# Optimization experiments

Measured on AMD Instinct MI355X. Metric: run time of the kernel, lower is better.

## Reference

```python
import jax, jax.numpy as jnp
import numpy as np

B, O, T = 32, 256, 1024
D_OBJ = 512      # obj_input_dim
D_PRED = 512     # predicate_input_dim
HID = 512        # hidden_dim
P_OUT = 512      # predicate_output_dim
OBJ_OUT = 512    # object_output_dim
N_PRED_TYPES = 50
ORIGINAL_EDGE = 0
TRANSITIVE_EDGE = 1


def setup_inputs() -> dict:
    key = jax.random.key(0)
    ks = jax.random.split(key, 16)

    def kaiming(k, fan_in, fan_out):
        return jax.random.normal(k, (fan_in, fan_out), jnp.float32) * np.sqrt(2.0 / fan_in)

    n1_in = 2 * D_OBJ + D_PRED            # 1536
    n1_out = 2 * HID + P_OUT              # 1536
    return {
        "obj_vecs": jax.random.normal(ks[0], (B, O, D_OBJ), jnp.float32),
        "pred_vecs": jax.random.normal(ks[1], (B, T, D_PRED), jnp.float32),
        "W1a": kaiming(ks[2], n1_in, HID), "b1a": jnp.zeros((HID,), jnp.float32),
        "W1b": kaiming(ks[3], HID, n1_out), "b1b": jnp.zeros((n1_out,), jnp.float32),
        "W2a": kaiming(ks[4], HID, HID), "b2a": jnp.zeros((HID,), jnp.float32),
        "W2b": kaiming(ks[5], HID, OBJ_OUT), "b2b": jnp.zeros((OBJ_OUT,), jnp.float32),
        "pt_weights": jax.random.normal(ks[6], (N_PRED_TYPES,), jnp.float32),
        "edges": jax.random.randint(ks[7], (B, T, 2), 0, O, jnp.int32),
        "pred_indicators": jax.random.randint(ks[8], (B, T), 0, 2, jnp.int32).astype(bool),
        "triplet_type": jax.random.randint(ks[9], (B, T), 0, 2, jnp.int32),
        "predicate_ids": jax.random.randint(ks[10], (B, T), 0, N_PRED_TYPES, jnp.int32),
    }


def reference(obj_vecs, pred_vecs, W1a, b1a, W1b, b1b, W2a, b2a, W2b, b2b,
              pt_weights, edges, pred_indicators, triplet_type, predicate_ids):
    s_idx = edges[:, :, 0]  # [B,T]
    o_idx = edges[:, :, 1]

    # gather subject/object vectors: [B,T,D]
    cur_s = jnp.take_along_axis(obj_vecs, s_idx[:, :, None], axis=1)
    cur_o = jnp.take_along_axis(obj_vecs, o_idx[:, :, None], axis=1)
    cur_t = jnp.concatenate([cur_s, pred_vecs, cur_o], axis=-1)  # [B,T,2D+Dp]

    # net1: Linear-ReLU-Linear-ReLU
    h = jax.nn.relu(cur_t @ W1a + b1a)
    new_t = jax.nn.relu(h @ W1b + b1b)  # [B,T,2*HID+P_OUT]

    # confidence weighting
    pt_pred = jax.nn.sigmoid(pt_weights)  # [N_PRED_TYPES]
    conf = ((triplet_type == ORIGINAL_EDGE).astype(jnp.float32)
            + (triplet_type == TRANSITIVE_EDGE).astype(jnp.float32) * pt_pred[predicate_ids])  # [B,T]
    new_t = new_t * conf[:, :, None]

    new_s = new_t[:, :, :HID]
    new_p = new_t[:, :, HID:HID + P_OUT]
    new_o = new_t[:, :, HID + P_OUT:]

    mask = pred_indicators.astype(jnp.float32)  # [B,T]

    def pool_one(si, oi, sv, ov, cf, m):
        # masked scatter-add (equivalent to torch boolean-masked scatter_add)
        sums = (jax.ops.segment_sum(sv * m[:, None], si, num_segments=O)
                + jax.ops.segment_sum(ov * m[:, None], oi, num_segments=O))  # [O,HID]
        w = cf * m
        counts = (jax.ops.segment_sum(w, si, num_segments=O)
                  + jax.ops.segment_sum(w, oi, num_segments=O))  # [O]
        nz = counts > 0
        return jnp.where(nz[:, None], sums / jnp.where(nz, counts, 1.0)[:, None], sums)

    pooled = jax.vmap(pool_one)(s_idx, o_idx, new_s, new_o, conf, mask)  # [B,O,HID]

    # net2: Linear-ReLU-Linear-ReLU
    h2 = jax.nn.relu(pooled @ W2a + b2a)
    new_obj = jax.nn.relu(h2 @ W2b + b2b)  # [B,O,OBJ_OUT]

    return new_obj, new_p
```

## Files before the change

kernel.cpp:

```cpp
#include <hip/hip_runtime.h>
#include <hip/hip_bf16.h>
#include <cstdint>
#include <cstddef>

#define DEV __device__ __forceinline__

typedef __attribute__((ext_vector_type(8))) short  s8v;
typedef __attribute__((ext_vector_type(4))) float  f4v;
typedef __attribute__((ext_vector_type(4))) uint32_t u4v;

DEV unsigned short f2bf(float x) {
  union { float f; uint32_t u; } v; v.f = x;
  uint32_t u = v.u + 0x7FFFu + ((v.u >> 16) & 1u);
  return (unsigned short)(u >> 16);
}
DEV uint32_t cvtpk2(float lo, float hi) {
  uint32_t r;
  asm("v_cvt_pk_bf16_f32 %0, %1, %2" : "=v"(r) : "v"(lo), "v"(hi));
  return r;
}
DEV unsigned short f2bf_fast(float x) { return (unsigned short)cvtpk2(x, 0.f); }
DEV float bf2f(unsigned short b) {
  union { uint32_t u; float f; } v; v.u = ((uint32_t)b) << 16;
  return v.f;
}

DEV void async_copy16(void* lds, const void* g) {
  typedef __attribute__((address_space(3))) uint32_t lds_t;
  typedef const __attribute__((address_space(1))) uint32_t g_t;
  __builtin_amdgcn_global_load_lds((g_t*)g, (lds_t*)lds, 16, 0, 0);
}

#define WAITV4()    asm volatile("s_waitcnt vmcnt(4)" ::: "memory")
#define WAITV0()    asm volatile("s_waitcnt vmcnt(0)" ::: "memory")
#define MEMFENCE()  asm volatile("" ::: "memory")

constexpr int Bc = 32, Oc = 256, Tc = 1024;
constexpr int BM = 128, BN = 128, BK = 64;
constexpr int CSR_CAP = 46;

DEV void swz_mn(int nyb, int* mb, int* nb) {
  const int nwg = gridDim.x * gridDim.y;
  const int w   = blockIdx.x + blockIdx.y * gridDim.x;
  const int cpx = nwg >> 3;
  const int s   = (w & 7) * cpx + (w >> 3);
  *mb = s / nyb;
  *nb = s % nyb;
}

__global__ __launch_bounds__(256)
void cvt_k(const float* __restrict__ in, unsigned short* __restrict__ outp, int n8)
{
  const int i = blockIdx.x * 256 + threadIdx.x;
  if (i >= n8) return;
  const f4v v0 = *(const f4v*)(in + (size_t)i * 8);
  const f4v v1 = *(const f4v*)(in + (size_t)i * 8 + 4);
  u4v pk;
  pk.x = cvtpk2(v0.x, v0.y);
  pk.y = cvtpk2(v0.z, v0.w);
  pk.z = cvtpk2(v1.x, v1.y);
  pk.w = cvtpk2(v1.z, v1.w);
  *(u4v*)(outp + (size_t)i * 8) = pk;
}

#define READ_A(QM, DST) do {                                                    \
    _Pragma("unroll")                                                           \
    for (int i = 0; i < 4; ++i) {                                               \
      const int row = wm * 128 + ((QM) * 4 + i) * 16 + (lane & 15);             \
      _Pragma("unroll")                                                         \
      for (int kk = 0; kk < 2; ++kk) {                                          \
        const int c = kk * 4 + (lane >> 4);                                     \
        DST[i][kk] = *(const s8v*)(Ab_ + row * 128 + ((c ^ (row & 7)) << 4));   \
      }                                                                         \
    }                                                                           \
  } while (0)

#define READ_B(QN, DST) do {                                                    \
    _Pragma("unroll")                                                           \
    for (int j = 0; j < 2; ++j) {                                               \
      const int row = wn * 64 + ((QN) * 2 + j) * 16 + (lane & 15);              \
      _Pragma("unroll")                                                         \
      for (int kk = 0; kk < 2; ++kk) {                                          \
        const int c = kk * 4 + (lane >> 4);                                     \
        DST[j][kk] = *(const s8v*)(Bb_ + row * 128 + ((c ^ (row & 7)) << 4));   \
      }                                                                         \
    }                                                                           \
  } while (0)

#define SYNC_MFMA(QM, QN, AF, BF) do {                                          \
    MEMFENCE();                                                                 \
    __builtin_amdgcn_s_barrier();                                               \
    asm volatile("s_waitcnt lgkmcnt(0)" ::: "memory");                          \
    __builtin_amdgcn_sched_barrier(0);                                          \
    __builtin_amdgcn_s_setprio(1);                                              \
    _Pragma("unroll")                                                           \
    for (int i = 0; i < 4; ++i)                                                 \
      _Pragma("unroll")                                                         \
      for (int j = 0; j < 2; ++j)                                               \
        _Pragma("unroll")                                                       \
        for (int kk = 0; kk < 2; ++kk)                                          \
          acc[(QM) * 4 + i][(QN) * 2 + j] =                                     \
            __builtin_amdgcn_mfma_f32_16x16x32_bf16(                            \
              AF[i][kk], BF[j][kk], acc[(QM) * 4 + i][(QN) * 2 + j], 0, 0, 0);  \
    __builtin_amdgcn_s_setprio(0);                                              \
  } while (0)

#define ENDPHASE() do { MEMFENCE(); __builtin_amdgcn_s_barrier(); } while (0)

#define KTILE_BODY() do {                                                       \
    const int par = t & 1, px = par ^ 1;                                        \
    const char* Ab_ = smem + par * 65536;                                       \
    const char* Bb_ = Ab_ + 32768;                                              \
    const bool s1 = (t + 1 < nk), s2 = (t + 2 < nk);                            \
                                                                        \
    READ_A(0, af); READ_B(0, bf0);                                              \
    if (s1) stageA(px, 1, t + 1);                                               \
    SYNC_MFMA(0, 0, af, bf0);                                                   \
    ENDPHASE();                                                                 \
                                                                        \
    READ_B(1, bf1);                                                             \
    if (s1) stageB(px, 1, t + 1);                                               \
    SYNC_MFMA(0, 1, af, bf1);                                                   \
    ENDPHASE();                                                                 \
                                                                        \
    READ_A(1, af);                                                              \
    if (s2) stageA(par, 0, t + 2);                                              \
    SYNC_MFMA(1, 1, af, bf1);                                                   \
    ENDPHASE();                                                                 \
                                                                        \
    if (s2) stageB(par, 0, t + 2);                                              \
    SYNC_MFMA(1, 0, af, bf0);                                                   \
    if (s2) { WAITV4(); } else if (s1) { WAITV0(); }                            \
    ENDPHASE();                                                                 \
  } while (0)

__global__ __launch_bounds__(512, 2)
void gemm8g_k(const unsigned short* __restrict__ objb,
              const unsigned short* __restrict__ predb,
              const int* __restrict__ edges,
              const unsigned short* __restrict__ Bt,
              const float* __restrict__ bias,
              unsigned short* __restrict__ outp)
{
  __shared__ __align__(16) char smem[131072];

  const int tid = threadIdx.x, lane = tid & 63, wave = tid >> 6;
  const int wm = wave >> 2, wn = wave & 3;
  int mb, nb; swz_mn(gridDim.y, &mb, &nb);
  const int m0 = mb * 256, n0 = nb * 256;
  const int rl  = tid >> 3;
  const int cs8 = ((lane & 7) ^ (lane >> 3)) * 8;
  const int rB0 = (rl >> 5) * 64 + (rl & 31);

  uint32_t offS[4], offP[4], offO[4];
  #pragma unroll
  for (int c2 = 0; c2 < 4; ++c2) {
    const int r = (c2 >> 1) * 128 + (c2 & 1) * 64 + rl;
    const int m = m0 + r;
    const int ob = (m >> 10) * Oc;
    offS[c2] = (uint32_t)((ob + edges[2 * m])     * 1024 + cs8 * 2);
    offO[c2] = (uint32_t)((ob + edges[2 * m + 1]) * 1024 + cs8 * 2);
    offP[c2] = (uint32_t)(m * 1024 + cs8 * 2);
  }
  const unsigned short* srcB = Bt + (size_t)(n0 + rB0) * 1536 + cs8;

  auto stageA = [&](int p, int qm, int kt) {
    const int reg = kt >> 3;
    const uint32_t koff = (uint32_t)(kt & 7) * 128u;
    #pragma unroll
    for (int s = 0; s < 2; ++s) {
      const int c2 = s * 2 + qm;
      const char* src;
      if (reg == 0)      src = (const char*)objb  + offS[c2] + koff;
      else if (reg == 1) src = (const char*)predb + offP[c2] + koff;
      else               src = (const char*)objb  + offO[c2] + koff;
      async_copy16(smem + p * 65536 + ((s * 128 + qm * 64 + wave * 8) << 7), src);
    }
  };
  auto stageB = [&](int p, int qn, int kt) {
    #pragma unroll
    for (int s = 0; s < 2; ++s)
      async_copy16(smem + p * 65536 + 32768 +
                     ((s * 128 + qn * 32 + (wave >> 2) * 64 + (wave & 3) * 8) << 7),
                   srcB + (size_t)(s * 128 + qn * 32) * 1536 + kt * 64);
  };

  f4v acc[8][4] = {};
  s8v af[4][2], bf0[2][2], bf1[2][2];
  constexpr int nk = 24;

  stageA(0, 0, 0); stageB(0, 0, 0); stageA(0, 1, 0); stageB(0, 1, 0);
  stageA(1, 0, 1); stageB(1, 0, 1);
  WAITV4();
  MEMFENCE();
  __builtin_amdgcn_s_barrier();

  for (int t = 0; t < nk; ++t) KTILE_BODY();

  const int cn = lane & 15, rq4 = (lane >> 4) * 4;
  #pragma unroll
  for (int f = 0; f < 8; ++f) {
    const int gr0 = m0 + wm * 128 + f * 16 + rq4;
    #pragma unroll
    for (int g = 0; g < 4; ++g) {
      const int gc = n0 + wn * 64 + g * 16 + cn;
      const float bv = bias[gc];
      #pragma unroll
      for (int r = 0; r < 4; ++r) {
        float val = acc[f][g][r] + bv;
        val = val > 0.f ? val : 0.f;
        outp[(size_t)(gr0 + r) * 512 + gc] = f2bf_fast(val);
      }
    }
  }
}

template<int EPI>
__global__ __launch_bounds__(256)
void gemm_k(const unsigned short* __restrict__ Abf,
            const unsigned short* __restrict__ Bt,
            const float* __restrict__ bias,
            const float* __restrict__ conf,
            unsigned short* __restrict__ out_bf,
            float* __restrict__ out_f32,
            int M, int N, int K)
{
  __shared__ __align__(16) char smem[BM * BK * 2 + BN * BK * 2];
  char* As = smem;
  char* Bs = smem + BM * BK * 2;

  const int tid  = threadIdx.x;
  const int lane = tid & 63;
  const int wave = tid >> 6;
  const int wm = wave >> 1, wn = wave & 1;
  int mb, nb; swz_mn(gridDim.y, &mb, &nb);
  const int m0 = mb * BM;
  const int n0 = nb * BN;

  f4v acc[4][4] = {};

  for (int k0 = 0; k0 < K; k0 += BK) {
    {
      const int r8 = lane >> 3;
      const int cs = (lane & 7) ^ r8;
      const unsigned short* src = Bt + (size_t)(n0 + wave * 32 + r8) * K + k0 + cs * 8;
      #pragma unroll
      for (int i = 0; i < 4; ++i)
        async_copy16(Bs + (wave * 32 + i * 8) * 128, src + (size_t)i * 8 * K);
      const unsigned short* srca = Abf + (size_t)(m0 + wave * 32 + r8) * K + k0 + cs * 8;
      #pragma unroll
      for (int i = 0; i < 4; ++i)
        async_copy16(As + (wave * 32 + i * 8) * 128, srca + (size_t)i * 8 * K);
    }
    __syncthreads();

    #pragma unroll
    for (int kk = 0; kk < 2; ++kk) {
      s8v af[4], bfv[4];
      #pragma unroll
      for (int i = 0; i < 4; ++i) {
        const int row = wm * 64 + i * 16 + (lane & 15);
        const int c = kk * 4 + (lane >> 4);
        af[i] = *(const s8v*)(As + row * 128 + ((c ^ (row & 7)) << 4));
      }
      #pragma unroll
      for (int j = 0; j < 4; ++j) {
        const int row = wn * 64 + j * 16 + (lane & 15);
        const int c = kk * 4 + (lane >> 4);
        bfv[j] = *(const s8v*)(Bs + row * 128 + ((c ^ (row & 7)) << 4));
      }
      #pragma unroll
      for (int i = 0; i < 4; ++i)
        #pragma unroll
        for (int j = 0; j < 4; ++j)
          acc[i][j] = __builtin_amdgcn_mfma_f32_16x16x32_bf16(af[i], bfv[j], acc[i][j], 0, 0, 0);
    }
    __syncthreads();
  }

  const int cn = lane & 15, rq4 = (lane >> 4) * 4;
  #pragma unroll
  for (int i = 0; i < 4; ++i) {
    const int gr0 = m0 + wm * 64 + i * 16 + rq4;
    #pragma unroll
    for (int j = 0; j < 4; ++j) {
      const int gc = n0 + wn * 64 + j * 16 + cn;
      const float bv = bias[gc];
      #pragma unroll
      for (int r = 0; r < 4; ++r) {
        float val = acc[i][j][r] + bv;
        val = val > 0.f ? val : 0.f;
        const int gr = gr0 + r;
        if (EPI == 0) out_bf[(size_t)gr * N + gc] = f2bf_fast(val);
        else if (EPI == 2) out_f32[(size_t)gr * N + gc] = val;
        else { out_f32[(size_t)gr * N + gc] = val * conf[gr]; }
      }
    }
  }
}

__global__ __launch_bounds__(256)
void gemm2so_k(const unsigned short* __restrict__ h,
               const int* __restrict__ torig,
               const float* __restrict__ confc,
               const unsigned short* __restrict__ W1bt,
               const float* __restrict__ b1b,
               const int* __restrict__ minfo,
               unsigned short* __restrict__ news_c,
               unsigned short* __restrict__ newo_c)
{
  const int Mp   = minfo[1];
  const int nact = (Mp >> 7) << 3;
  const int w    = blockIdx.x + blockIdx.y * gridDim.x;
  if (w >= nact) return;
  const int cpx = nact >> 3;
  const int s   = (w & 7) * cpx + (w >> 3);
  const int mb  = s >> 3, nb = s & 7;
  const int m0  = mb * BM;
  const int Mr  = minfo[0];

  __shared__ __align__(16) char smem[BM * BK * 2 + BN * BK * 2];
  char* As = smem;
  char* Bs = smem + BM * BK * 2;

  const int tid  = threadIdx.x;
  const int lane = tid & 63;
  const int wave = tid >> 6;
  const int wm = wave >> 1, wn = wave & 1;
  const int n0 = nb * BN;
  const int r8 = lane >> 3;
  const int cs8 = ((lane & 7) ^ r8) * 8;

  const unsigned short* aP[4];
  #pragma unroll
  for (int i = 0; i < 4; ++i) {
    int m = m0 + wave * 32 + i * 8 + r8;
    m = m < Mr ? m : Mr - 1;
    aP[i] = h + (size_t)torig[m] * 512 + cs8;
  }
  const int nrow0 = (nb < 4) ? n0 : n0 + 512;
  const unsigned short* bsrc = W1bt + (size_t)(nrow0 + wave * 32 + r8) * 512 + cs8;

  f4v acc[4][4] = {};

  for (int kt = 0; kt < 8; ++kt) {
    const int kin = kt * 64;
    #pragma unroll
    for (int i = 0; i < 4; ++i)
      async_copy16(Bs + (wave * 32 + i * 8) * 128, bsrc + (size_t)(i * 8) * 512 + kin);
    #pragma unroll
    for (int i = 0; i < 4; ++i)
      async_copy16(As + (wave * 32 + i * 8) * 128, aP[i] + kin);
    __syncthreads();

    #pragma unroll
    for (int kk = 0; kk < 2; ++kk) {
      s8v af[4], bfv[4];
      #pragma unroll
      for (int i = 0; i < 4; ++i) {
        const int row = wm * 64 + i * 16 + (lane & 15);
        const int c = kk * 4 + (lane >> 4);
        af[i] = *(const s8v*)(As + row * 128 + ((c ^ (row & 7)) << 4));
      }
      #pragma unroll
      for (int j = 0; j < 4; ++j) {
        const int row = wn * 64 + j * 16 + (lane & 15);
        const int c = kk * 4 + (lane >> 4);
        bfv[j] = *(const s8v*)(Bs + row * 128 + ((c ^ (row & 7)) << 4));
      }
      #pragma unroll
      for (int i = 0; i < 4; ++i)
        #pragma unroll
        for (int j = 0; j < 4; ++j)
          acc[i][j] = __builtin_amdgcn_mfma_f32_16x16x32_bf16(af[i], bfv[j], acc[i][j], 0, 0, 0);
    }
    __syncthreads();
  }

  const float* bb = b1b + ((nb < 4) ? n0 : 512 + n0);
  unsigned short* outp = (nb < 4) ? news_c : newo_c;
  const int c0 = (nb & 3) * 128;
  const int cn = lane & 15, rq4 = (lane >> 4) * 4;
  #pragma unroll
  for (int i = 0; i < 4; ++i) {
    const int gr0 = m0 + wm * 64 + i * 16 + rq4;
    #pragma unroll
    for (int j = 0; j < 4; ++j) {
      const int lc = wn * 64 + j * 16 + cn;
      const float bv = bb[lc];
      #pragma unroll
      for (int r = 0; r < 4; ++r) {
        const int gr = gr0 + r;
        float val = acc[i][j][r] + bv;
        val = val > 0.f ? val : 0.f;
        val *= confc[gr < Mr ? gr : 0];
        if (gr < Mr) outp[(size_t)gr * 512 + c0 + lc] = f2bf_fast(val);
      }
    }
  }
}

__global__ void tcvt_k(const float* __restrict__ W, unsigned short* __restrict__ Wt,
                       int K, int N)
{
  __shared__ float tile[32][33];
  const int k0 = blockIdx.x * 32, n0 = blockIdx.y * 32;
  const int tx = threadIdx.x, ty = threadIdx.y;
  #pragma unroll
  for (int i = 0; i < 32; i += 8)
    tile[ty + i][tx] = W[(size_t)(k0 + ty + i) * N + (n0 + tx)];
  __syncthreads();
  #pragma unroll
  for (int i = 0; i < 32; i += 8)
    Wt[(size_t)(n0 + ty + i) * K + (k0 + tx)] = f2bf(tile[tx][ty + i]);
}

__global__ void detect_k(const unsigned char* __restrict__ mb, int* __restrict__ flag)
{
  __shared__ int any;
  if (threadIdx.x == 0) any = 0;
  __syncthreads();
  int local = 0;
  for (int i = threadIdx.x; i < Bc * Tc; i += 256)
    if ((i & 3) && mb[i]) local = 1;
  if (local) atomicOr(&any, 1);
  __syncthreads();
  if (threadIdx.x == 0) *flag = any;
}

__global__ void prep_k(const int* __restrict__ tt, const int* __restrict__ pid,
                       const float* __restrict__ ptw, const int* __restrict__ edges,
                       const void* __restrict__ mask, const int* __restrict__ u8flag,
                       float* __restrict__ conf, int* __restrict__ se,
                       int* __restrict__ oe)
{
  const int m = blockIdx.x * 256 + threadIdx.x;
  const int t = tt[m];
  float c = 0.f;
  if (t == 0) c = 1.f;
  else if (t == 1) c = 1.f / (1.f + expf(-ptw[pid[m]]));
  conf[m] = c;
  bool mk;
  if (*u8flag) mk = ((const unsigned char*)mask)[m] != 0;
  else         mk = ((const int*)mask)[m] != 0;
  se[m] = mk ? edges[2 * m]     : -1;
  oe[m] = mk ? edges[2 * m + 1] : -1;
}

__global__ __launch_bounds__(1024)
void scan1_k(const int* __restrict__ se, int* __restrict__ bsum)
{
  const int m = blockIdx.x * 1024 + threadIdx.x;
  const unsigned long long bal = __ballot(se[m] >= 0);
  __shared__ int wc[16];
  if ((threadIdx.x & 63) == 0) wc[threadIdx.x >> 6] = (int)__popcll(bal);
  __syncthreads();
  if (threadIdx.x == 0) {
    int s = 0;
    #pragma unroll
    for (int i = 0; i < 16; ++i) s += wc[i];
    bsum[blockIdx.x] = s;
  }
}

__global__ void scan2_k(const int* __restrict__ bsum, int* __restrict__ boff,
                        int* __restrict__ minfo)
{
  if (threadIdx.x == 0) {
    int s = 0;
    for (int i = 0; i < 32; ++i) { boff[i] = s; s += bsum[i]; }
    minfo[0] = s;
    minfo[1] = (s + 127) & ~127;
  }
}

__global__ __launch_bounds__(1024)
void scan3_k(const int* __restrict__ se, const int* __restrict__ boff,
             const float* __restrict__ conf,
             int* __restrict__ torig, int* __restrict__ cmap,
             float* __restrict__ confc)
{
  const int m = blockIdx.x * 1024 + threadIdx.x;
  const int lane = threadIdx.x & 63, w = threadIdx.x >> 6;
  const bool mv = se[m] >= 0;
  const unsigned long long bal = __ballot(mv);
  __shared__ int wc[16];
  if (lane == 0) wc[w] = (int)__popcll(bal);
  __syncthreads();
  int woff = 0;
  for (int i = 0; i < w; ++i) woff += wc[i];
  if (mv) {
    const int c = boff[blockIdx.x] + woff +
                  (int)__popcll(bal & ((1ull << lane) - 1ull));
    torig[c] = m;
    cmap[m]  = c;
    confc[c] = conf[m];
  }
}

__global__ __launch_bounds__(256)
void csr2_k(const int* __restrict__ se, const int* __restrict__ oe,
            int* __restrict__ deg, int* __restrict__ slot)
{
  const int wid  = blockIdx.x * 4 + (threadIdx.x >> 6);
  const int b    = wid >> 8;
  const int u    = wid & 255;
  const int lane = threadIdx.x & 63;
  const int mb   = b * Tc;
  int* sl = slot + (size_t)wid * CSR_CAP;
  const unsigned long long lt = (1ull << lane) - 1ull;
  int cnt = 0;
  #pragma unroll 4
  for (int c = 0; c < 16; ++c) {
    const int t = c * 64 + lane;
    const int s = se[mb + t];
    const int o = oe[mb + t];
    const unsigned long long ms = __ballot(s == u);
    const unsigned long long mo = __ballot(o == u);
    if (s == u) {
      const int pos = cnt + (int)__popcll(ms & lt);
      if (pos < CSR_CAP) sl[pos] = 2 * t;
    }
    cnt += (int)__popcll(ms);
    if (o == u) {
      const int pos = cnt + (int)__popcll(mo & lt);
      if (pos < CSR_CAP) sl[pos] = 2 * t + 1;
    }
    cnt += (int)__popcll(mo);
  }
  if (lane == 0) deg[wid] = cnt < CSR_CAP ? cnt : CSR_CAP;
}

__global__ __launch_bounds__(256)
void pool2_k(const unsigned short* __restrict__ S, const unsigned short* __restrict__ Ov,
             const int* __restrict__ deg, const int* __restrict__ slot,
             const float* __restrict__ conf, const int* __restrict__ cmap,
             unsigned short* __restrict__ pooled)
{
  const int bo = blockIdx.x;
  const int b  = bo >> 8;
  const int u  = threadIdx.x;
  const int d  = deg[bo];
  const int* sl = slot + (size_t)bo * CSR_CAP;
  float a0 = 0.f, a1 = 0.f, w = 0.f;
  for (int i = 0; i < d; ++i) {
    const int e = sl[i];
    const int t = e >> 1;
    const int c = cmap[b * Tc + t];
    const unsigned short* row = ((e & 1) ? Ov : S) + (size_t)c * 512;
    const uint32_t pr = *(const uint32_t*)(row + 2 * u);
    a0 += bf2f((unsigned short)pr);
    a1 += bf2f((unsigned short)(pr >> 16));
    w  += conf[b * Tc + t];
  }
  const float denom = (w > 0.f) ? w : 1.f;
  const size_t ob = (size_t)bo * 512;
  *(uint32_t*)(pooled + ob + 2 * u) = cvtpk2(a0 / denom, a1 / denom);
}

extern "C" void kernel_launch(void* const* d_in, const int* in_sizes, int n_in,
                              void* d_out, int out_size, void* d_ws, size_t ws_size,
                              hipStream_t stream)
{
  const float* obj  = (const float*)d_in[0];
  const float* pred = (const float*)d_in[1];
  const float* W1a  = (const float*)d_in[2];
  const float* b1a  = (const float*)d_in[3];
  const float* W1b  = (const float*)d_in[4];
  const float* b1b  = (const float*)d_in[5];
  const float* W2a  = (const float*)d_in[6];
  const float* b2a  = (const float*)d_in[7];
  const float* W2b  = (const float*)d_in[8];
  const float* b2b  = (const float*)d_in[9];
  const float* ptw  = (const float*)d_in[10];
  const int*   edges = (const int*)d_in[11];
  const void*  mask  = d_in[12];
  const int*   tt    = (const int*)d_in[13];
  const int*   pid   = (const int*)d_in[14];
  float* out = (float*)d_out;

  char* ws = (char*)d_ws;
  unsigned short* W1at = (unsigned short*)(ws + 0);
  unsigned short* W1bt = (unsigned short*)(ws + 1572864);
  unsigned short* W2at = (unsigned short*)(ws + 3145728);
  unsigned short* W2bt = (unsigned short*)(ws + 3670016);
  int* deg  = (int*)(ws + 0);
  int* slot = (int*)(ws + 32768);
  unsigned short* h    = (unsigned short*)(ws + 4194304);
  unsigned short* pooled = h;
  unsigned short* h2   = (unsigned short*)(ws + 12582912);
  unsigned short* news = (unsigned short*)(ws + 37748736);
  unsigned short* newo = (unsigned short*)(ws + 71303168);
  unsigned short* objb = news;
  unsigned short* predb = (unsigned short*)(ws + 46137344);
  float* conf = (float*)(ws + 104857600);
  int*   se   = (int*)(ws + 104988672);
  int*   oe   = (int*)(ws + 105119744);
  int* u8flag = (int*)(ws + 105250816);

  char* sout = (char*)d_out;
  int*   torig = (int*)(sout + 0);
  int*   cmap  = (int*)(sout + 131072);
  float* confc = (float*)(sout + 262144);
  int*   bsum  = (int*)(sout + 393216);
  int*   boff  = (int*)(sout + 393344);
  int*   minfo = (int*)(sout + 393472);

  tcvt_k<<<dim3(48, 16), dim3(32, 8), 0, stream>>>(W1a, W1at, 1536, 512);
  tcvt_k<<<dim3(16, 48), dim3(32, 8), 0, stream>>>(W1b, W1bt, 512, 1536);
  tcvt_k<<<dim3(16, 16), dim3(32, 8), 0, stream>>>(W2a, W2at, 512, 512);
  tcvt_k<<<dim3(16, 16), dim3(32, 8), 0, stream>>>(W2b, W2bt, 512, 512);

  cvt_k<<<2048, 256, 0, stream>>>(obj,  objb,  Bc * Oc * 512 / 8);
  cvt_k<<<8192, 256, 0, stream>>>(pred, predb, Bc * Tc * 512 / 8);

  detect_k<<<1, 256, 0, stream>>>((const unsigned char*)mask, u8flag);
  prep_k<<<128, 256, 0, stream>>>(tt, pid, ptw, edges, mask, u8flag, conf, se, oe);

  scan1_k<<<32, 1024, 0, stream>>>(se, bsum);
  scan2_k<<<1, 64, 0, stream>>>(bsum, boff, minfo);
  scan3_k<<<32, 1024, 0, stream>>>(se, boff, conf, torig, cmap, confc);

  gemm8g_k<<<dim3(128, 2), 512, 0, stream>>>(objb, predb, edges, W1at, b1a, h);

  csr2_k<<<2048, 256, 0, stream>>>(se, oe, deg, slot);

  gemm_k<3><<<dim3(256, 4), 256, 0, stream>>>(
      h, W1bt + 512 * 512, b1b + 512, conf, nullptr, out + 4194304, 32768, 512, 512);

  gemm2so_k<<<dim3(256, 8), 256, 0, stream>>>(
      h, torig, confc, W1bt, b1b, minfo, news, newo);

  pool2_k<<<Bc * Oc, 256, 0, stream>>>(news, newo, deg, slot, conf, cmap, pooled);

  gemm_k<0><<<dim3(64, 4), 256, 0, stream>>>(
      pooled, W2at, b2a, nullptr, h2, nullptr, 8192, 512, 512);

  gemm_k<2><<<dim3(64, 4), 256, 0, stream>>>(
      h2, W2bt, b2b, nullptr, nullptr, out, 8192, 512, 512);
}
```

Measured before the change: 254.5 us.

## Precompute per-object projections to shrink first-layer GEMM from K=1536 to K=512

The first linear layer is split algebraically. The subject and object parts of W1a are applied once per object (8192 rows) in a separate GEMM that writes fp32 projections into scratch output space. A new fused GEMM then handles only the predicate part (K=512) and adds the gathered subject and object projections plus bias in its epilogue. This removes the gathered K=1536 GEMM over 32768 rows, but adds an extra kernel, fp32 gathers in the epilogue, and a simpler single-buffered GEMM in place of the hand-pipelined one.

```diff
diff --git a/kernel.cpp b/kernel.cpp
--- a/kernel.cpp
+++ b/kernel.cpp
@@ -30,10 +30,6 @@
   typedef const __attribute__((address_space(1))) uint32_t g_t;
   __builtin_amdgcn_global_load_lds((g_t*)g, (lds_t*)lds, 16, 0, 0);
 }
-
-#define WAITV4()    asm volatile("s_waitcnt vmcnt(4)" ::: "memory")
-#define WAITV0()    asm volatile("s_waitcnt vmcnt(0)" ::: "memory")
-#define MEMFENCE()  asm volatile("" ::: "memory")
 
 constexpr int Bc = 32, Oc = 256, Tc = 1024;
 constexpr int BM = 128, BN = 128, BK = 64;
@@ -63,158 +59,6 @@
   *(u4v*)(outp + (size_t)i * 8) = pk;
 }
 
-#define READ_A(QM, DST) do {                                                    \
-    _Pragma("unroll")                                                           \
-    for (int i = 0; i < 4; ++i) {                                               \
-      const int row = wm * 128 + ((QM) * 4 + i) * 16 + (lane & 15);             \
-      _Pragma("unroll")                                                         \
-      for (int kk = 0; kk < 2; ++kk) {                                          \
-        const int c = kk * 4 + (lane >> 4);                                     \
-        DST[i][kk] = *(const s8v*)(Ab_ + row * 128 + ((c ^ (row & 7)) << 4));   \
-      }                                                                         \
-    }                                                                           \
-  } while (0)
-
-#define READ_B(QN, DST) do {                                                    \
-    _Pragma("unroll")                                                           \
-    for (int j = 0; j < 2; ++j) {                                               \
-      const int row = wn * 64 + ((QN) * 2 + j) * 16 + (lane & 15);              \
-      _Pragma("unroll")                                                         \
-      for (int kk = 0; kk < 2; ++kk) {                                          \
-        const int c = kk * 4 + (lane >> 4);                                     \
-        DST[j][kk] = *(const s8v*)(Bb_ + row * 128 + ((c ^ (row & 7)) << 4));   \
-      }                                                                         \
-    }                                                                           \
-  } while (0)
-
-#define SYNC_MFMA(QM, QN, AF, BF) do {                                          \
-    MEMFENCE();                                                                 \
-    __builtin_amdgcn_s_barrier();                                               \
-    asm volatile("s_waitcnt lgkmcnt(0)" ::: "memory");                          \
-    __builtin_amdgcn_sched_barrier(0);                                          \
-    __builtin_amdgcn_s_setprio(1);                                              \
-    _Pragma("unroll")                                                           \
-    for (int i = 0; i < 4; ++i)                                                 \
-      _Pragma("unroll")                                                         \
-      for (int j = 0; j < 2; ++j)                                               \
-        _Pragma("unroll")                                                       \
-        for (int kk = 0; kk < 2; ++kk)                                          \
-          acc[(QM) * 4 + i][(QN) * 2 + j] =                                     \
-            __builtin_amdgcn_mfma_f32_16x16x32_bf16(                            \
-              AF[i][kk], BF[j][kk], acc[(QM) * 4 + i][(QN) * 2 + j], 0, 0, 0);  \
-    __builtin_amdgcn_s_setprio(0);                                              \
-  } while (0)
-
-#define ENDPHASE() do { MEMFENCE(); __builtin_amdgcn_s_barrier(); } while (0)
-
-#define KTILE_BODY() do {                                                       \
-    const int par = t & 1, px = par ^ 1;                                        \
-    const char* Ab_ = smem + par * 65536;                                       \
-    const char* Bb_ = Ab_ + 32768;                                              \
-    const bool s1 = (t + 1 < nk), s2 = (t + 2 < nk);                            \
-                                                                        \
-    READ_A(0, af); READ_B(0, bf0);                                              \
-    if (s1) stageA(px, 1, t + 1);                                               \
-    SYNC_MFMA(0, 0, af, bf0);                                                   \
-    ENDPHASE();                                                                 \
-                                                                        \
-    READ_B(1, bf1);                                                             \
-    if (s1) stageB(px, 1, t + 1);                                               \
-    SYNC_MFMA(0, 1, af, bf1);                                                   \
-    ENDPHASE();                                                                 \
-                                                                        \
-    READ_A(1, af);                                                              \
-    if (s2) stageA(par, 0, t + 2);                                              \
-    SYNC_MFMA(1, 1, af, bf1);                                                   \
-    ENDPHASE();                                                                 \
-                                                                        \
-    if (s2) stageB(par, 0, t + 2);                                              \
-    SYNC_MFMA(1, 0, af, bf0);                                                   \
-    if (s2) { WAITV4(); } else if (s1) { WAITV0(); }                            \
-    ENDPHASE();                                                                 \
-  } while (0)
-
-__global__ __launch_bounds__(512, 2)
-void gemm8g_k(const unsigned short* __restrict__ objb,
-              const unsigned short* __restrict__ predb,
-              const int* __restrict__ edges,
-              const unsigned short* __restrict__ Bt,
-              const float* __restrict__ bias,
-              unsigned short* __restrict__ outp)
-{
-  __shared__ __align__(16) char smem[131072];
-
-  const int tid = threadIdx.x, lane = tid & 63, wave = tid >> 6;
-  const int wm = wave >> 2, wn = wave & 3;
-  int mb, nb; swz_mn(gridDim.y, &mb, &nb);
-  const int m0 = mb * 256, n0 = nb * 256;
-  const int rl  = tid >> 3;
-  const int cs8 = ((lane & 7) ^ (lane >> 3)) * 8;
-  const int rB0 = (rl >> 5) * 64 + (rl & 31);
-
-  uint32_t offS[4], offP[4], offO[4];
-  #pragma unroll
-  for (int c2 = 0; c2 < 4; ++c2) {
-    const int r = (c2 >> 1) * 128 + (c2 & 1) * 64 + rl;
-    const int m = m0 + r;
-    const int ob = (m >> 10) * Oc;
-    offS[c2] = (uint32_t)((ob + edges[2 * m])     * 1024 + cs8 * 2);
-    offO[c2] = (uint32_t)((ob + edges[2 * m + 1]) * 1024 + cs8 * 2);
-    offP[c2] = (uint32_t)(m * 1024 + cs8 * 2);
-  }
-  const unsigned short* srcB = Bt + (size_t)(n0 + rB0) * 1536 + cs8;
-
-  auto stageA = [&](int p, int qm, int kt) {
-    const int reg = kt >> 3;
-    const uint32_t koff = (uint32_t)(kt & 7) * 128u;
-    #pragma unroll
-    for (int s = 0; s < 2; ++s) {
-      const int c2 = s * 2 + qm;
-      const char* src;
-      if (reg == 0)      src = (const char*)objb  + offS[c2] + koff;
-      else if (reg == 1) src = (const char*)predb + offP[c2] + koff;
-      else               src = (const char*)objb  + offO[c2] + koff;
-      async_copy16(smem + p * 65536 + ((s * 128 + qm * 64 + wave * 8) << 7), src);
-    }
-  };
-  auto stageB = [&](int p, int qn, int kt) {
-    #pragma unroll
-    for (int s = 0; s < 2; ++s)
-      async_copy16(smem + p * 65536 + 32768 +
-                     ((s * 128 + qn * 32 + (wave >> 2) * 64 + (wave & 3) * 8) << 7),
-                   srcB + (size_t)(s * 128 + qn * 32) * 1536 + kt * 64);
-  };
-
-  f4v acc[8][4] = {};
-  s8v af[4][2], bf0[2][2], bf1[2][2];
-  constexpr int nk = 24;
-
-  stageA(0, 0, 0); stageB(0, 0, 0); stageA(0, 1, 0); stageB(0, 1, 0);
-  stageA(1, 0, 1); stageB(1, 0, 1);
-  WAITV4();
-  MEMFENCE();
-  __builtin_amdgcn_s_barrier();
-
-  for (int t = 0; t < nk; ++t) KTILE_BODY();
-
-  const int cn = lane & 15, rq4 = (lane >> 4) * 4;
-  #pragma unroll
-  for (int f = 0; f < 8; ++f) {
-    const int gr0 = m0 + wm * 128 + f * 16 + rq4;
-    #pragma unroll
-    for (int g = 0; g < 4; ++g) {
-      const int gc = n0 + wn * 64 + g * 16 + cn;
-      const float bv = bias[gc];
-      #pragma unroll
-      for (int r = 0; r < 4; ++r) {
-        float val = acc[f][g][r] + bv;
-        val = val > 0.f ? val : 0.f;
-        outp[(size_t)(gr0 + r) * 512 + gc] = f2bf_fast(val);
-      }
-    }
-  }
-}
-
 template<int EPI>
 __global__ __launch_bounds__(256)
 void gemm_k(const unsigned short* __restrict__ Abf,
@@ -285,15 +129,102 @@
     #pragma unroll
     for (int j = 0; j < 4; ++j) {
       const int gc = n0 + wn * 64 + j * 16 + cn;
-      const float bv = bias[gc];
+      const float bv = (EPI == 4) ? 0.f : bias[gc];
       #pragma unroll
       for (int r = 0; r < 4; ++r) {
-        float val = acc[i][j][r] + bv;
+        const int gr = gr0 + r;
+        if (EPI == 4) {
+          out_f32[(size_t)gr * N + gc] = acc[i][j][r];
+        } else {
+          float val = acc[i][j][r] + bv;
+          val = val > 0.f ? val : 0.f;
+          if (EPI == 0)      out_bf[(size_t)gr * N + gc] = f2bf_fast(val);
+          else if (EPI == 2) out_f32[(size_t)gr * N + gc] = val;
+          else               out_f32[(size_t)gr * N + gc] = val * conf[gr];
+        }
+      }
+    }
+  }
+}
+
+__global__ __launch_bounds__(256)
+void gemm1f_k(const unsigned short* __restrict__ predb,
+              const unsigned short* __restrict__ W1amt,
+              const float* __restrict__ b1a,
+              const float* __restrict__ objP,
+              const int* __restrict__ edges,
+              unsigned short* __restrict__ h)
+{
+  __shared__ __align__(16) char smem[BM * BK * 2 + BN * BK * 2];
+  char* As = smem;
+  char* Bs = smem + BM * BK * 2;
+
+  const int tid  = threadIdx.x;
+  const int lane = tid & 63;
+  const int wave = tid >> 6;
+  const int wm = wave >> 1, wn = wave & 1;
+  int mb, nb; swz_mn(gridDim.y, &mb, &nb);
+  const int m0 = mb * BM;
+  const int n0 = nb * BN;
+
+  f4v acc[4][4] = {};
+
+  for (int k0 = 0; k0 < 512; k0 += BK) {
+    {
+      const int r8 = lane >> 3;
+      const int cs = (lane & 7) ^ r8;
+      const unsigned short* src = W1amt + (size_t)(n0 + wave * 32 + r8) * 512 + k0 + cs * 8;
+      #pragma unroll
+      for (int i = 0; i < 4; ++i)
+        async_copy16(Bs + (wave * 32 + i * 8) * 128, src + (size_t)i * 8 * 512);
+      const unsigned short* srca = predb + (size_t)(m0 + wave * 32 + r8) * 512 + k0 + cs * 8;
+      #pragma unroll
+      for (int i = 0; i < 4; ++i)
+        async_copy16(As + (wave * 32 + i * 8) * 128, srca + (size_t)i * 8 * 512);
+    }
+    __syncthreads();
+
+    #pragma unroll
+    for (int kk = 0; kk < 2; ++kk) {
+      s8v af[4], bfv[4];
+      #pragma unroll
+      for (int i = 0; i < 4; ++i) {
+        const int row = wm * 64 + i * 16 + (lane & 15);
+        const int c = kk * 4 + (lane >> 4);
+        af[i] = *(const s8v*)(As + row * 128 + ((c ^ (row & 7)) << 4));
+      }
+      #pragma unroll
+      for (int j = 0; j < 4; ++j) {
+        const int row = wn * 64 + j * 16 + (lane & 15);
+        const int c = kk * 4 + (lane >> 4);
+        bfv[j] = *(const s8v*)(Bs + row * 128 + ((c ^ (row & 7)) << 4));
+      }
+      #pragma unroll
+      for (int i = 0; i < 4; ++i)
+        #pragma unroll
+        for (int j = 0; j < 4; ++j)
+          acc[i][j] = __builtin_amdgcn_mfma_f32_16x16x32_bf16(af[i], bfv[j], acc[i][j], 0, 0, 0);
+    }
+    __syncthreads();
+  }
+
+  const int cn = lane & 15, rq4 = (lane >> 4) * 4;
+  #pragma unroll
+  for (int i = 0; i < 4; ++i) {
+    const int gr0 = m0 + wm * 64 + i * 16 + rq4;
+    #pragma unroll
+    for (int r = 0; r < 4; ++r) {
+      const int gr = gr0 + r;
+      const int ob = (gr >> 10) * Oc;
+      const int es = edges[2 * gr], eo = edges[2 * gr + 1];
+      const float* pS = objP + (size_t)(ob + es) * 1024;
+      const float* pO = objP + (size_t)(ob + eo) * 1024 + 512;
+      #pragma unroll
+      for (int j = 0; j < 4; ++j) {
+        const int gc = n0 + wn * 64 + j * 16 + cn;
+        float val = acc[i][j][r] + b1a[gc] + pS[gc] + pO[gc];
         val = val > 0.f ? val : 0.f;
-        const int gr = gr0 + r;
-        if (EPI == 0) out_bf[(size_t)gr * N + gc] = f2bf_fast(val);
-        else if (EPI == 2) out_f32[(size_t)gr * N + gc] = val;
-        else { out_f32[(size_t)gr * N + gc] = val * conf[gr]; }
+        h[(size_t)gr * 512 + gc] = f2bf_fast(val);
       }
     }
   }
@@ -580,10 +511,11 @@
   float* out = (float*)d_out;
 
   char* ws = (char*)d_ws;
-  unsigned short* W1at = (unsigned short*)(ws + 0);
-  unsigned short* W1bt = (unsigned short*)(ws + 1572864);
-  unsigned short* W2at = (unsigned short*)(ws + 3145728);
-  unsigned short* W2bt = (unsigned short*)(ws + 3670016);
+  unsigned short* WPt   = (unsigned short*)(ws + 0);
+  unsigned short* W1amt = (unsigned short*)(ws + 1048576);
+  unsigned short* W1bt  = (unsigned short*)(ws + 1572864);
+  unsigned short* W2at  = (unsigned short*)(ws + 3145728);
+  unsigned short* W2bt  = (unsigned short*)(ws + 3670016);
   int* deg  = (int*)(ws + 0);
   int* slot = (int*)(ws + 32768);
   unsigned short* h    = (unsigned short*)(ws + 4194304);
@@ -605,8 +537,11 @@
   int*   bsum  = (int*)(sout + 393216);
   int*   boff  = (int*)(sout + 393344);
   int*   minfo = (int*)(sout + 393472);
-
-  tcvt_k<<<dim3(48, 16), dim3(32, 8), 0, stream>>>(W1a, W1at, 1536, 512);
+  float* objP  = out + 4194304;
+
+  tcvt_k<<<dim3(16, 16), dim3(32, 8), 0, stream>>>(W1a, WPt, 512, 512);
+  tcvt_k<<<dim3(16, 16), dim3(32, 8), 0, stream>>>(W1a + 1024 * 512, WPt + 512 * 512, 512, 512);
+  tcvt_k<<<dim3(16, 16), dim3(32, 8), 0, stream>>>(W1a + 512 * 512, W1amt, 512, 512);
   tcvt_k<<<dim3(16, 48), dim3(32, 8), 0, stream>>>(W1b, W1bt, 512, 1536);
   tcvt_k<<<dim3(16, 16), dim3(32, 8), 0, stream>>>(W2a, W2at, 512, 512);
   tcvt_k<<<dim3(16, 16), dim3(32, 8), 0, stream>>>(W2b, W2bt, 512, 512);
@@ -621,7 +556,10 @@
   scan2_k<<<1, 64, 0, stream>>>(bsum, boff, minfo);
   scan3_k<<<32, 1024, 0, stream>>>(se, boff, conf, torig, cmap, confc);
 
-  gemm8g_k<<<dim3(128, 2), 512, 0, stream>>>(objb, predb, edges, W1at, b1a, h);
+  gemm_k<4><<<dim3(64, 8), 256, 0, stream>>>(
+      objb, WPt, nullptr, nullptr, nullptr, objP, 8192, 1024, 512);
+
+  gemm1f_k<<<dim3(256, 4), 256, 0, stream>>>(predb, W1amt, b1a, objP, edges, h);
 
   csr2_k<<<2048, 256, 0, stream>>>(se, oe, deg, slot);
 
```

Measured after the change: 263.0 us. 1.03x slower.
